# Performance work log

Hardware: AMD Instinct MI355X
Metric: run time of the kernel (lower is better)

## Reference

```python
import jax, jax.numpy as jnp
import numpy as np

N, T, CIN = 40000, 32, 8
VW = 64          # back_voxelwise_channels
P = 16           # v2b_maxvoxels (voxels stacked per BEV cell)
BEV_H, BEV_W = 496, 432
EPS = 1e-5


def _bn(key, shape):
    # returns stacked (gamma, beta, running_mean, running_var) along axis -2
    k1, k2, k3 = jax.random.split(key, 3)
    g = 1.0 + 0.1 * jax.random.normal(k1, shape, jnp.float32)
    b = 0.1 * jax.random.normal(k2, shape, jnp.float32)
    m = 0.1 * jax.random.normal(k3, shape, jnp.float32)
    v = jnp.ones(shape, jnp.float32)
    return jnp.stack([g, b, m, v], axis=-2)


def setup_inputs() -> dict:
    key = jax.random.key(0)
    ks = jax.random.split(key, 20)
    features = jax.random.normal(ks[0], (N, T, CIN), jnp.float32)
    cy = jax.random.randint(ks[1], (N, 1), 0, BEV_H)
    cx = jax.random.randint(ks[2], (N, 1), 0, BEV_W)
    coors = jnp.concatenate([cy, cx], axis=1).astype(jnp.int32)
    num_voxels = jax.random.randint(ks[3], (N,), 1, T + 1).astype(jnp.int32)

    def w(k, o, i):
        return jax.random.normal(k, (o, i), jnp.float32) / float(np.sqrt(i))

    return dict(
        features=features, coors=coors, num_voxels=num_voxels,
        vfe1_W=w(ks[4], 8, CIN), vfe1_bn=_bn(ks[5], (8,)),
        vfe2_W=w(ks[6], 32, 16), vfe2_bn=_bn(ks[7], (32,)),
        vfe3_W=w(ks[8], 64, 64), vfe3_bn=_bn(ks[9], (64,)),
        vfe4_W=w(ks[10], 64, 64), vfe4_bn=_bn(ks[11], (64,)),
        bfe1_W=jax.random.normal(ks[12], (16, P, P), jnp.float32) / float(np.sqrt(P)),
        bfe1_bn=_bn(ks[13], (16, P)),
        bfe2_W=jax.random.normal(ks[14], (16, 2, P), jnp.float32) / float(np.sqrt(P)),
        bfe2_bn=_bn(ks[15], (16, 2)),
        bfe3_W=w(ks[16], 128, 128), bfe3_bn=_bn(ks[17], (128,)),
    )


def _forward(features, vfe1_W, vfe1_bn, vfe2_W, vfe2_bn, vfe3_W, vfe3_bn,
             vfe4_W, vfe4_bn, bfe1_W, bfe1_bn, bfe2_W, bfe2_bn, bfe3_W, bfe3_bn,
             coors, num_voxels):
    n, t = features.shape[0], features.shape[1]
    f32 = features.dtype
    mask = (jnp.arange(t)[None, :] < num_voxels[:, None]).astype(f32)[..., None]  # [N,T,1]

    def fe(x, W, bn):  # Linear (no bias) + BatchNorm1d (eval) + Mish
        g, b, m, v = bn
        y = x @ W.T
        y = (y - m) * jax.lax.rsqrt(v + EPS) * g + b
        return y * jnp.tanh(jax.nn.softplus(y))

    def vfe(x, W, bn):  # pointwise FE, max-pool over points, concat
        p = fe(x, W, bn)
        agg = jnp.max(p, axis=1, keepdims=True)
        return jnp.concatenate([p, jnp.broadcast_to(agg, p.shape)], axis=2)

    x1 = vfe(features, vfe1_W, vfe1_bn)           # [N,T,16]
    x2 = vfe(x1, vfe2_W, vfe2_bn) * mask          # [N,T,64]
    x3 = fe(x2, vfe3_W, vfe3_bn)
    x4 = fe(x3, vfe4_W, vfe4_bn) * mask + x2
    voxelwise = jnp.max(x4, axis=1)               # [N,64]

    # ---- voxel2bev: group voxels by BEV cell, stack up to P per cell ----
    cell = coors[:, 0] * BEV_W + coors[:, 1]                         # [N]
    ucell, inv = jnp.unique(cell, return_inverse=True, size=n, fill_value=BEV_H * BEV_W)
    order = jnp.argsort(inv)                                          # stable
    inv_sorted = inv[order]
    pos_sorted = jnp.arange(n) - jnp.searchsorted(inv_sorted, inv_sorted, side='left')
    slot = jnp.zeros(n, jnp.int32).at[order].set(pos_sorted.astype(jnp.int32))
    row = jnp.where(slot < P, inv, n)                                 # overflow -> dropped
    bevs = jnp.zeros((n, P, VW), f32).at[row, jnp.minimum(slot, P - 1)].set(
        voxelwise, mode='drop')                                       # [N,P,64]
    counts = jax.ops.segment_sum(jnp.ones(n, jnp.int32), inv, num_segments=n)
    numv = jnp.minimum(counts, P)
    bevcoors = jnp.stack([ucell // BEV_W, ucell % BEV_W], axis=1)     # [N,2]

    # ---- 16 grouped FE stacks over the slot dimension ----
    x0 = bevs.transpose(0, 2, 1).reshape(n, 16, 4, P)                 # [N,16,4,P]
    m2 = (jnp.arange(P)[None, :] < numv[:, None]).astype(f32)[:, None, None, :]
    y = jnp.einsum('ngip,gqp->ngiq', x0, bfe1_W)                      # [N,16,4,P]
    g1, b1, m1, v1 = (bfe1_bn[None, :, i, None, :] for i in range(4))
    y = (y - m1) * jax.lax.rsqrt(v1 + EPS) * g1 + b1
    y = y * jnp.tanh(jax.nn.softplus(y)) * m2
    z = jnp.einsum('ngip,gcp->ngic', y, bfe2_W)                       # [N,16,4,2]
    g2, b2, m2b, v2 = (bfe2_bn[None, :, i, None, :] for i in range(4))
    z = (z - m2b) * jax.lax.rsqrt(v2 + EPS) * g2 + b2
    z = z * jnp.tanh(jax.nn.softplus(z))
    # torch cat along dim=-1 then view -> layout [N, 4, 16, 2] flattened
    x17 = z.transpose(0, 2, 1, 3).reshape(n, 128)
    x18 = fe(x17, bfe3_W, bfe3_bn)
    x19 = fe(x18, bfe3_W, bfe3_bn)   # original applies bfe3 twice (bfe4 unused)

    bevmap = jnp.zeros((BEV_H, BEV_W, 128), f32).at[
        bevcoors[:, 0], bevcoors[:, 1]].set(x19, mode='drop')
    return bevmap.transpose(2, 1, 0)                                  # [128, W, H]


def reference(features, coors, num_voxels, vfe1_W, vfe1_bn, vfe2_W, vfe2_bn,
              vfe3_W, vfe3_bn, vfe4_W, vfe4_bn, bfe1_W, bfe1_bn, bfe2_W, bfe2_bn,
              bfe3_W, bfe3_bn):
    return _forward(features, vfe1_W, vfe1_bn, vfe2_W, vfe2_bn, vfe3_W, vfe3_bn,
                    vfe4_W, vfe4_bn, bfe1_W, bfe1_bn, bfe2_W, bfe2_bn,
                    bfe3_W, bfe3_bn, coors, num_voxels)
```

## Files before the change

kernel.cpp:

```cpp
#include <hip/hip_runtime.h>

#define BEVW 432
#define BEVH 496
#define NCELL (BEVW*BEVH)
#define NVOX  40000
#define EPSB  1e-5f

typedef float f32x2 __attribute__((ext_vector_type(2)));
typedef float f32x4 __attribute__((ext_vector_type(4)));
typedef unsigned int u32x4 __attribute__((ext_vector_type(4)));
typedef short bf16x8 __attribute__((ext_vector_type(8)));

#define REP8_0(M)  M(0) M(1) M(2) M(3) M(4) M(5) M(6) M(7)
#define REP8_8(M)  M(8) M(9) M(10) M(11) M(12) M(13) M(14) M(15)
#define REP8_16(M) M(16) M(17) M(18) M(19) M(20) M(21) M(22) M(23)
#define REP8_24(M) M(24) M(25) M(26) M(27) M(28) M(29) M(30) M(31)
#define REP16_0(M)  REP8_0(M)  REP8_8(M)
#define REP32_0(M) REP16_0(M) REP8_16(M) REP8_24(M)


__device__ __forceinline__ float mishf(float y) {
    float e = __expf(fminf(y, 40.f));
    float n = e * (e + 2.f);
    return y * n * __builtin_amdgcn_rcpf(n + 2.f);
}

template <int CTRL>
__device__ __forceinline__ float dppmaxf(float a) {
    int p = __builtin_amdgcn_update_dpp(0, __float_as_int(a), CTRL, 0xF, 0xF, true);
    return fmaxf(a, __int_as_float(p));
}
#define WMAX32(a) { \
    a = dppmaxf<0xB1>(a); \
    a = dppmaxf<0x4E>(a); \
    a = dppmaxf<0x141>(a); \
    a = dppmaxf<0x140>(a); \
    a = fmaxf(a, __int_as_float(__builtin_amdgcn_ds_swizzle(__float_as_int(a), 0x401F))); }

__device__ __forceinline__ bf16x8 mkbf8(uint a, uint b, uint c, uint d) {
    u32x4 t = {a, b, c, d};
    return __builtin_bit_cast(bf16x8, t);
}

__device__ __forceinline__ uint splitbf(float x) {
    uint rh = __float_as_uint(x) & 0xFFFF0000u;
    float lof = x - __uint_as_float(rh);
    uint ul = __float_as_uint(lof);
    uint rl = (ul + 0x7FFFu + ((ul >> 16) & 1u)) >> 16;
    return (rh >> 16) | (rl << 16);
}

__global__ __launch_bounds__(256) void setup_kernel(
    const float* __restrict__ vbn1, const float* __restrict__ vbn2,
    const float* __restrict__ vbn3, const float* __restrict__ vbn4,
    const float* __restrict__ bbn1, const float* __restrict__ bbn2,
    const float* __restrict__ bbn3, const float* __restrict__ W4,
    const float* __restrict__ W3g,
    float* __restrict__ fold, ushort* __restrict__ w4fh, ushort* __restrict__ w4fl,
    ushort* __restrict__ w3fh, ushort* __restrict__ w3fl)
{
    int tid = threadIdx.x;
    if (tid < 8)  { float s = vbn1[tid]/sqrtf(vbn1[24+tid]+EPSB);  fold[tid]      = s; fold[8+tid]   = vbn1[8+tid]  - vbn1[16+tid]*s; }
    if (tid < 32) { float s = vbn2[tid]/sqrtf(vbn2[96+tid]+EPSB);  fold[16+tid]   = s; fold[48+tid]  = vbn2[32+tid] - vbn2[64+tid]*s; }
    if (tid < 64) { float s = vbn3[tid]/sqrtf(vbn3[192+tid]+EPSB); fold[80+tid]   = s; fold[144+tid] = vbn3[64+tid] - vbn3[128+tid]*s; }
    if (tid < 64) { float s = vbn4[tid]/sqrtf(vbn4[192+tid]+EPSB); fold[208+tid]  = s; fold[272+tid] = vbn4[64+tid] - vbn4[128+tid]*s; }
    if (tid < 128){ float s = bbn3[tid]/sqrtf(bbn3[384+tid]+EPSB); fold[336+tid]  = s; fold[464+tid] = bbn3[128+tid]- bbn3[256+tid]*s; }
    { int g = tid >> 4, q = tid & 15;
      const float* b = bbn1 + g*64;
      float s = b[q]/sqrtf(b[48+q]+EPSB);
      fold[592+tid] = s; fold[848+tid] = b[16+q] - b[32+q]*s; }
    if (tid < 32) { int g = tid >> 1, c = tid & 1;
      const float* b = bbn2 + g*8;
      float s = b[c]/sqrtf(b[6+c]+EPSB);
      fold[1104+tid] = s; fold[1136+tid] = b[2+c] - b[4+c]*s; }

    for (int i = tid; i < 4096; i += 256) {
        int j = i & 7, ln = (i >> 3) & 63, nt = (i >> 9) & 3, kc = i >> 11;
        int n = (ln & 15) + nt*16;
        int k = kc*32 + (ln >> 4)*8 + j;
        {
            float val = W4[n*64 + k];
            uint rh = __float_as_uint(val) & 0xFFFF0000u;
            float lof = val - __uint_as_float(rh);
            uint ul = __float_as_uint(lof);
            uint rl = (ul + 0x7FFFu + ((ul >> 16) & 1u)) >> 16;
            w4fh[i] = (ushort)(rh >> 16);
            w4fl[i] = (ushort)rl;
        }
        {
            float val = W3g[n*64 + k];
            uint rh = __float_as_uint(val) & 0xFFFF0000u;
            float lof = val - __uint_as_float(rh);
            uint ul = __float_as_uint(lof);
            uint rl = (ul + 0x7FFFu + ((ul >> 16) & 1u)) >> 16;
            w3fh[i] = (ushort)(rh >> 16);
            w3fl[i] = (ushort)rl;
        }
    }
}

#define PAIRS(M) M(0,0,1) M(1,2,3) M(2,4,5) M(3,6,7) M(4,8,9) M(5,10,11) \
  M(6,12,13) M(7,14,15) M(8,16,17) M(9,18,19) M(10,20,21) M(11,22,23) \
  M(12,24,25) M(13,26,27) M(14,28,29) M(15,30,31)

#define MF3(D, AH, AL, BH, BL) \
    D = __builtin_amdgcn_mfma_f32_16x16x32_bf16(AL, BH, D, 0, 0, 0); \
    D = __builtin_amdgcn_mfma_f32_16x16x32_bf16(AH, BL, D, 0, 0, 0); \
    D = __builtin_amdgcn_mfma_f32_16x16x32_bf16(AH, BH, D, 0, 0, 0);

#define LDA(SRCP, mt, AH, AL) { \
    const uint* ap_ = (SRCP) + ((lane & 15) + 16*(mt))*33 + quad*8; \
    uint u0 = ap_[0], u1 = ap_[1], u2 = ap_[2], u3 = ap_[3]; \
    uint u4 = ap_[4], u5 = ap_[5], u6 = ap_[6], u7 = ap_[7]; \
    AH = mkbf8(__builtin_amdgcn_perm(u1,u0,0x05040100), __builtin_amdgcn_perm(u3,u2,0x05040100), \
               __builtin_amdgcn_perm(u5,u4,0x05040100), __builtin_amdgcn_perm(u7,u6,0x05040100)); \
    AL = mkbf8(__builtin_amdgcn_perm(u1,u0,0x07060302), __builtin_amdgcn_perm(u3,u2,0x07060302), \
               __builtin_amdgcn_perm(u5,u4,0x07060302), __builtin_amdgcn_perm(u7,u6,0x07060302)); }

#define TILE4(SRCP, mt, D0, D1, D2, D3) { \
    bf16x8 Ah_, Al_; LDA(SRCP, mt, Ah_, Al_) \
    MF3(D0, Ah_, Al_, B0h_, B0l_) MF3(D1, Ah_, Al_, B1h_, B1l_) \
    MF3(D2, Ah_, Al_, B2h_, B2l_) MF3(D3, Ah_, Al_, B3h_, B3l_) }

#define DOSET(SRCP, BHP, BLP, ACC, SKA, SKB) { \
    uint4 h0_=(BHP)[0], l0_=(BLP)[0], h1_=(BHP)[64], l1_=(BLP)[64]; \
    uint4 h2_=(BHP)[128], l2_=(BLP)[128], h3_=(BHP)[192], l3_=(BLP)[192]; \
    bf16x8 B0h_=mkbf8(h0_.x,h0_.y,h0_.z,h0_.w), B0l_=mkbf8(l0_.x,l0_.y,l0_.z,l0_.w); \
    bf16x8 B1h_=mkbf8(h1_.x,h1_.y,h1_.z,h1_.w), B1l_=mkbf8(l1_.x,l1_.y,l1_.z,l1_.w); \
    bf16x8 B2h_=mkbf8(h2_.x,h2_.y,h2_.z,h2_.w), B2l_=mkbf8(l2_.x,l2_.y,l2_.z,l2_.w); \
    bf16x8 B3h_=mkbf8(h3_.x,h3_.y,h3_.z,h3_.w), B3l_=mkbf8(l3_.x,l3_.y,l3_.z,l3_.w); \
    TILE4(SRCP, 0, ACC[0], ACC[1], ACC[2], ACC[3]) \
    TILE4(SRCP, 2, ACC[8], ACC[9], ACC[10], ACC[11]) \
    if (!(SKA)) { TILE4(SRCP, 1, ACC[4], ACC[5], ACC[6], ACC[7]) } \
    if (!(SKB)) { TILE4(SRCP, 3, ACC[12], ACC[13], ACC[14], ACC[15]) } }

__global__ __launch_bounds__(64, 3) void vfe_kernel(
    const float* __restrict__ feat, const int* __restrict__ coors,
    const int* __restrict__ nvx,
    const float* __restrict__ W1, const float* __restrict__ W2,
    const ushort* __restrict__ w3fh, const ushort* __restrict__ w3fl,
    const ushort* __restrict__ w4fh, const ushort* __restrict__ w4fl,
    const float* __restrict__ fold,
    float* __restrict__ voxelwise, int* __restrict__ cnt,
    int* __restrict__ list, int* __restrict__ nact, int* __restrict__ act)
{
    __shared__ char ldsbuf[17152];
    int tid = threadIdx.x;
    int lane = tid;
    int quad = lane >> 4;
    int v = blockIdx.x * 2 + (tid >> 5);
    int vA = blockIdx.x * 2;
    int t = tid & 31;
    uint*  x2s  = (uint*)ldsbuf;
    float* aggL = (float*)(ldsbuf + 16896);

    const float* fp = feat + (v*32 + t)*8;
    float4 fa = *(const float4*)fp;
    float4 fb = *(const float4*)(fp+4);
    int numv = nvx[v];
    float maskf = (t < numv) ? 1.f : 0.f;

#define D1(o) float x1_##o; float m1_##o;
    REP8_0(D1)
#undef D1
#define FE1(o) { const float* w = W1 + (o)*8; \
    float ya = fa.x*w[0] + fa.y*w[1]; float yb = fa.z*w[2] + fa.w*w[3]; \
    float yc = fb.x*w[4] + fb.y*w[5]; float yd = fb.z*w[6] + fb.w*w[7]; \
    float yy = ((ya+yb)+(yc+yd)) * fold[(o)] + fold[8+(o)]; \
    x1_##o = mishf(yy); }
    REP8_0(FE1)
#undef FE1
#define P1(o) { float a = x1_##o; WMAX32(a); m1_##o = a; }
    REP8_0(P1)
#undef P1

    f32x2 x1p_0 = {x1_0,x1_1}, x1p_1 = {x1_2,x1_3}, x1p_2 = {x1_4,x1_5}, x1p_3 = {x1_6,x1_7};
    f32x2 m1p_0 = {m1_0,m1_1}, m1p_1 = {m1_2,m1_3}, m1p_2 = {m1_4,m1_5}, m1p_3 = {m1_6,m1_7};

#define D2(o) float x2_##o; float agg_##o;
    REP32_0(D2)
#undef D2
#define FE2(o) { const f32x2* wp = (const f32x2*)(W2 + (o)*16); \
    f32x2 sa = x1p_0*wp[0]; sa += x1p_1*wp[1]; \
    f32x2 sb = x1p_2*wp[2]; sb += x1p_3*wp[3]; \
    f32x2 sc = m1p_0*wp[4]; sc += m1p_1*wp[5]; \
    f32x2 sd = m1p_2*wp[6]; sd += m1p_3*wp[7]; \
    sa += sb; sc += sd; sa += sc; \
    float yy = (sa.x + sa.y) * fold[16+(o)] + fold[48+(o)]; \
    x2_##o = mishf(yy); }
    REP32_0(FE2)
#undef FE2
#define P2(o) { float a = x2_##o; WMAX32(a); agg_##o = a; }
    REP32_0(P2)
#undef P2

#define PX(i,a,b) f32x2 x2p_##i = {x2_##a, x2_##b}; f32x2 aggp_##i = {agg_##a, agg_##b};
    PAIRS(PX)
#undef PX

    f32x2 maskp = {maskf, maskf};
#define MSK(i) x2p_##i *= maskp; aggp_##i *= maskp;
    REP16_0(MSK)
#undef MSK

    if (t == 0) {
        float* ag = aggL + (lane >> 5)*32;
#define AGW(i) ag[2*(i)] = aggp_##i.x; ag[2*(i)+1] = aggp_##i.y;
        REP16_0(AGW)
#undef AGW
    }

    int nA = __builtin_amdgcn_readfirstlane(__shfl(numv, 0));
    int nB = __builtin_amdgcn_readfirstlane(__shfl(numv, 32));
    const bool skipA = (nA <= 16);
    const bool skipB = (nB <= 16);

#define X2W(i) { \
    x2s[lane*33 + 2*(i)]          = splitbf(x2p_##i.x); \
    x2s[lane*33 + 2*(i)+1]        = splitbf(x2p_##i.y); \
    x2s[2112 + lane*33 + 2*(i)]   = splitbf(aggp_##i.x); \
    x2s[2112 + lane*33 + 2*(i)+1] = splitbf(aggp_##i.y); }
    REP16_0(X2W)
#undef X2W

    f32x4 e[16];
#define EIN(i) e[i] = (f32x4){0.f,0.f,0.f,0.f};
    REP16_0(EIN)
#undef EIN
    {
        const uint4* bh3 = (const uint4*)w3fh + lane;
        const uint4* bl3 = (const uint4*)w3fl + lane;
        DOSET(x2s, bh3, bl3, e, skipA, skipB)
    }
    {
        const uint4* bh3 = (const uint4*)w3fh + 256 + lane;
        const uint4* bl3 = (const uint4*)w3fl + 256 + lane;
        const uint* sp = x2s + 2112;
        DOSET(sp, bh3, bl3, e, skipA, skipB)
    }

    int c0 = lane & 15;
    uint* x3st = x2s + 2112;
    f32x4 d[16];
#define DIN(i) d[i] = (f32x4){0.f,0.f,0.f,0.f};
    REP16_0(DIN)
#undef DIN

#define POST(TI, mt, nt) { \
    float s_ = fold[80 + c0 + 16*(nt)], tb_ = fold[144 + c0 + 16*(nt)]; \
    int col_ = c0 + 16*((nt)&1); \
    int rowb_ = quad*4 + 16*(mt); \
    x3st[(rowb_+0)*33 + col_] = splitbf(mishf(e[TI].x * s_ + tb_)); \
    x3st[(rowb_+1)*33 + col_] = splitbf(mishf(e[TI].y * s_ + tb_)); \
    x3st[(rowb_+2)*33 + col_] = splitbf(mishf(e[TI].z * s_ + tb_)); \
    x3st[(rowb_+3)*33 + col_] = splitbf(mishf(e[TI].w * s_ + tb_)); }

    {
        POST(0,0,0)  POST(1,0,1)
        POST(8,2,0)  POST(9,2,1)
        if (!skipA) { POST(4,1,0)  POST(5,1,1) }
        if (!skipB) { POST(12,3,0) POST(13,3,1) }
        const uint4* bh4 = (const uint4*)w4fh + lane;
        const uint4* bl4 = (const uint4*)w4fl + lane;
        DOSET(x3st, bh4, bl4, d, skipA, skipB)
    }
    {
        POST(2,0,2)  POST(3,0,3)
        POST(10,2,2) POST(11,2,3)
        if (!skipA) { POST(6,1,2)  POST(7,1,3) }
        if (!skipB) { POST(14,3,2) POST(15,3,3) }
        const uint4* bh4 = (const uint4*)w4fh + 256 + lane;
        const uint4* bl4 = (const uint4*)w4fl + 256 + lane;
        DOSET(x3st, bh4, bl4, d, skipA, skipB)
    }
#undef POST

    float s0f = fold[208+c0],    t0f = fold[272+c0];
    float s1f = fold[208+16+c0], t1f = fold[272+16+c0];
    float s2f = fold[208+32+c0], t2f = fold[272+32+c0];
    float s3f = fold[208+48+c0], t3f = fold[272+48+c0];
    float rA2 = aggL[c0],      rA3 = aggL[16+c0];
    float rB2 = aggL[32+c0],   rB3 = aggL[48+c0];
    float piA = skipA ? 0.f : -3.4e38f;
    float piB = skipB ? 0.f : -3.4e38f;
    float pA0=piA, pA1=piA, pA2=piA, pA3=piA;
    float pB0=piB, pB1=piB, pB2=piB, pB3=piB;

#define RECON(u) (__uint_as_float((u)<<16) + __uint_as_float((u) & 0xFFFF0000u))
#define FTP(D, mt, nt, SS, TT, PV) { \
    int nv = ((mt) >> 1) ? nB : nA; \
    int rf = quad*4 + 16*(mt); \
    int rt = quad*4 + 16*((mt)&1); \
    int cb = c0 + 16*(nt); \
    float m0=(rt+0<nv)?1.f:0.f, m1=(rt+1<nv)?1.f:0.f, m2=(rt+2<nv)?1.f:0.f, m3=(rt+3<nv)?1.f:0.f; \
    uint ua_ = x2s[(rf+0)*33 + cb], ub_ = x2s[(rf+1)*33 + cb]; \
    uint uc_ = x2s[(rf+2)*33 + cb], ud_ = x2s[(rf+3)*33 + cb]; \
    float y0 = mishf(D.x*SS + TT)*m0 + RECON(ua_); \
    float y1 = mishf(D.y*SS + TT)*m1 + RECON(ub_); \
    float y2 = mishf(D.z*SS + TT)*m2 + RECON(uc_); \
    float y3 = mishf(D.w*SS + TT)*m3 + RECON(ud_); \
    PV = fmaxf(PV, fmaxf(fmaxf(y0,y1), fmaxf(y2,y3))); }

#define FTA(D, mt, nt, SS, TT, AG, PV) { \
    int nv = ((mt) >> 1) ? nB : nA; \
    int rt = quad*4 + 16*((mt)&1); \
    float m0=(rt+0<nv)?1.f:0.f, m1=(rt+1<nv)?1.f:0.f, m2=(rt+2<nv)?1.f:0.f, m3=(rt+3<nv)?1.f:0.f; \
    float y0 = (mishf(D.x*SS + TT) + AG)*m0; \
    float y1 = (mishf(D.y*SS + TT) + AG)*m1; \
    float y2 = (mishf(D.z*SS + TT) + AG)*m2; \
    float y3 = (mishf(D.w*SS + TT) + AG)*m3; \
    PV = fmaxf(PV, fmaxf(fmaxf(y0,y1), fmaxf(y2,y3))); }

    FTP(d[0], 0, 0, s0f, t0f, pA0)  FTP(d[1], 0, 1, s1f, t1f, pA1)
    FTA(d[2], 0, 2, s2f, t2f, rA2, pA2)  FTA(d[3], 0, 3, s3f, t3f, rA3, pA3)
    if (!skipA) {
        FTP(d[4], 1, 0, s0f, t0f, pA0)  FTP(d[5], 1, 1, s1f, t1f, pA1)
        FTA(d[6], 1, 2, s2f, t2f, rA2, pA2)  FTA(d[7], 1, 3, s3f, t3f, rA3, pA3)
    }
    FTP(d[8], 2, 0, s0f, t0f, pB0)  FTP(d[9], 2, 1, s1f, t1f, pB1)
    FTA(d[10], 2, 2, s2f, t2f, rB2, pB2)  FTA(d[11], 2, 3, s3f, t3f, rB3, pB3)
    if (!skipB) {
        FTP(d[12], 3, 0, s0f, t0f, pB0)  FTP(d[13], 3, 1, s1f, t1f, pB1)
        FTA(d[14], 3, 2, s2f, t2f, rB2, pB2)  FTA(d[15], 3, 3, s3f, t3f, rB3, pB3)
    }
#undef FTP
#undef FTA
#undef RECON

#define RED(p) p = fmaxf(p, __shfl_xor(p, 16)); p = fmaxf(p, __shfl_xor(p, 32));
    RED(pA0) RED(pA1) RED(pA2) RED(pA3) RED(pB0) RED(pB1) RED(pB2) RED(pB3)
#undef RED

    if (quad == 0) {
        float* vwA = voxelwise + vA*64;
        vwA[c0] = pA0; vwA[c0+16] = pA1; vwA[c0+32] = pA2; vwA[c0+48] = pA3;
        float* vwB = voxelwise + (vA+1)*64;
        vwB[c0] = pB0; vwB[c0+16] = pB1; vwB[c0+32] = pB2; vwB[c0+48] = pB3;
    }

    if (t == 0) {
        int cell = coors[v*2] * BEVW + coors[v*2+1];
        int pos = atomicAdd(&cnt[cell], 1);
        if (pos < 16) list[cell*16 + pos] = v;
        if (pos == 0) { int k = atomicAdd(nact, 1); act[k] = cell; }
    }
}

__global__ __launch_bounds__(256) void bfe_front(
    const int* __restrict__ nact, const int* __restrict__ act,
    const int* __restrict__ cnt, const int* __restrict__ list,
    const float* __restrict__ voxelwise,
    const float* __restrict__ W1g, const float* __restrict__ W2g,
    const float* __restrict__ fold, float* __restrict__ x17g,
    int* __restrict__ idx)
{
    int n_act = *nact;
    int aidx = blockIdx.x * 4 + (threadIdx.x >> 6);
    if (aidx >= n_act) return;

    int lane = threadIdx.x & 63;
    int g = lane >> 2, ii = lane & 3;
    int cell = act[aidx];
    int numv = min(cnt[cell], 16);
    if (lane == 0) idx[cell] = aidx + 1;

    int myidx = (lane < numv) ? list[cell*16 + lane] : (0x40000000 + lane);
    int rank = 0;
    for (int j = 0; j < numv; j++) { int vj = __shfl(myidx, j); rank += (vj < myidx) ? 1 : 0; }
    if (lane >= numv) rank = lane;
    int sorted = __builtin_amdgcn_ds_permute(rank << 2, myidx);

#define YD(q) float y_##q = 0.f;
    REP16_0(YD)
#undef YD
    for (int p = 0; p < numv; p++) {
        int sv = __shfl(sorted, p);
        float val = voxelwise[sv*64 + lane];
        const float* w = W1g + g*256 + p;
#define BF1(q) y_##q += val * w[(q)*16];
        REP16_0(BF1)
#undef BF1
    }
#define BN1(q) { float yy = y_##q * fold[592 + g*16 + (q)] + fold[848 + g*16 + (q)]; \
    yy = mishf(yy); y_##q = ((q) < numv) ? yy : 0.f; }
    REP16_0(BN1)
#undef BN1

    float z0 = 0.f, z1 = 0.f;
#define BF2(p) z0 += y_##p * W2g[g*32 + (p)]; z1 += y_##p * W2g[g*32 + 16 + (p)];
    REP16_0(BF2)
#undef BF2
    z0 = mishf(z0 * fold[1104 + g*2 + 0] + fold[1136 + g*2 + 0]);
    z1 = mishf(z1 * fold[1104 + g*2 + 1] + fold[1136 + g*2 + 1]);

    int k0 = ii*32 + g*2;
    *(float2*)(x17g + aidx*128 + k0) = make_float2(z0, z1);
}

__global__ __launch_bounds__(512, 4) void bfe3_fused(
    const int* __restrict__ nactp,
    const float* __restrict__ W3, const float* __restrict__ fold,
    float* __restrict__ x17g)
{
    __shared__ float XL[64*128];
    int tid = threadIdx.x;
    int n_act = *nactp;
    int cb = blockIdx.x * 64;

    for (int i = tid; i < 64*32; i += 512) {
        int c = i >> 5, kc = i & 31;
        float4 val = (cb + c < n_act) ? ((const float4*)x17g)[(size_t)(cb+c)*32 + kc]
                                      : make_float4(0.f,0.f,0.f,0.f);
        ((float4*)XL)[c*32 + (kc ^ (c & 31))] = val;
    }
    __syncthreads();

    int wv = __builtin_amdgcn_readfirstlane(tid >> 6);
    int c  = tid & 63;
    int ob = wv * 16;
    int cswz = c & 31;
    const float4* xrow = (const float4*)XL + c*32;
    const float4* W4p = (const float4*)W3;

#define DECLB(q) f32x2 ap_##q = {0.f, 0.f};
#define ACCB(q) { const f32x2* wp_ = (const f32x2*)(W4p + (ob+(q))*32 + kc); \
    ap_##q += xv01 * wp_[0]; ap_##q += xv23 * wp_[1]; }
#define ACTB(q) float a_##q; { float yy = (ap_##q.x + ap_##q.y) * fold[336+ob+(q)] + fold[464+ob+(q)]; a_##q = mishf(yy); }
    {
        REP16_0(DECLB)
        for (int kc = 0; kc < 32; kc++) {
            float4 xv = xrow[kc ^ cswz];
            f32x2 xv01 = {xv.x, xv.y}, xv23 = {xv.z, xv.w};
            REP16_0(ACCB)
        }
        REP16_0(ACTB)
        __syncthreads();
        ((float4*)XL)[c*32 + ((wv*4 + 0) ^ cswz)] = make_float4(a_0,  a_1,  a_2,  a_3);
        ((float4*)XL)[c*32 + ((wv*4 + 1) ^ cswz)] = make_float4(a_4,  a_5,  a_6,  a_7);
        ((float4*)XL)[c*32 + ((wv*4 + 2) ^ cswz)] = make_float4(a_8,  a_9,  a_10, a_11);
        ((float4*)XL)[c*32 + ((wv*4 + 3) ^ cswz)] = make_float4(a_12, a_13, a_14, a_15);
    }
    __syncthreads();

    {
        const float4* yrow = (const float4*)XL + c*32;
        REP16_0(DECLB)
        for (int kc = 0; kc < 32; kc++) {
            float4 xv = yrow[kc ^ cswz];
            f32x2 xv01 = {xv.x, xv.y}, xv23 = {xv.z, xv.w};
            REP16_0(ACCB)
        }
        REP16_0(ACTB)
        float4* dst = (float4*)(x17g + (size_t)(cb + c)*128 + ob);
        dst[0] = make_float4(a_0,  a_1,  a_2,  a_3);
        dst[1] = make_float4(a_4,  a_5,  a_6,  a_7);
        dst[2] = make_float4(a_8,  a_9,  a_10, a_11);
        dst[3] = make_float4(a_12, a_13, a_14, a_15);
    }
#undef DECLB
#undef ACCB
#undef ACTB
}

__global__ __launch_bounds__(512, 2) void bev_write(
    const int* __restrict__ idx, const float* __restrict__ x19c,
    float* __restrict__ out)
{
    __shared__ float XT[128*65];
    int bid = blockIdx.x;
    int cx = bid % BEVW;
    int cy0 = (bid / BEVW) << 6;
    int tid = threadIdx.x;

    int cell_l = tid >> 3;
    int chq = (tid & 7) << 4;
    int cy = cy0 + cell_l;
    float4 v0 = make_float4(0.f,0.f,0.f,0.f), v1 = v0, v2 = v0, v3 = v0;
    if (cy < BEVH) {
        int ai = idx[cy*BEVW + cx] - 1;
        if (ai >= 0) {
            const float4* src = (const float4*)(x19c + (size_t)ai*128 + chq);
            v0 = src[0]; v1 = src[1]; v2 = src[2]; v3 = src[3];
        }
    }
    float* d = XT + chq*65 + cell_l;
    d[0*65]=v0.x;  d[1*65]=v0.y;  d[2*65]=v0.z;  d[3*65]=v0.w;
    d[4*65]=v1.x;  d[5*65]=v1.y;  d[6*65]=v1.z;  d[7*65]=v1.w;
    d[8*65]=v2.x;  d[9*65]=v2.y;  d[10*65]=v2.z; d[11*65]=v2.w;
    d[12*65]=v3.x; d[13*65]=v3.y; d[14*65]=v3.z; d[15*65]=v3.w;
    __syncthreads();

    int wv2 = tid >> 6, lane = tid & 63;
    int cyw = cy0 + lane;
    if (cyw < BEVH) {
        float* op = out + cx*BEVH + cyw;
#pragma unroll
        for (int k = 0; k < 16; k++) {
            int c = (wv2 << 4) + k;
            op[(size_t)c*NCELL] = XT[c*65 + lane];
        }
    }
}

extern "C" void kernel_launch(void* const* d_in, const int* in_sizes, int n_in,
                              void* d_out, int out_size, void* d_ws, size_t ws_size,
                              hipStream_t stream) {
    const float* features = (const float*)d_in[0];
    const int*   coors    = (const int*)d_in[1];
    const int*   num_vox  = (const int*)d_in[2];
    const float* vfe1_W   = (const float*)d_in[3];
    const float* vfe1_bn  = (const float*)d_in[4];
    const float* vfe2_W   = (const float*)d_in[5];
    const float* vfe2_bn  = (const float*)d_in[6];
    const float* vfe3_W   = (const float*)d_in[7];
    const float* vfe3_bn  = (const float*)d_in[8];
    const float* vfe4_W   = (const float*)d_in[9];
    const float* vfe4_bn  = (const float*)d_in[10];
    const float* bfe1_W   = (const float*)d_in[11];
    const float* bfe1_bn  = (const float*)d_in[12];
    const float* bfe2_W   = (const float*)d_in[13];
    const float* bfe2_bn  = (const float*)d_in[14];
    const float* bfe3_W   = (const float*)d_in[15];
    const float* bfe3_bn  = (const float*)d_in[16];
    float* out = (float*)d_out;

    char* ws = (char*)d_ws;
    int*    nact      = (int*)ws;
    int*    cnt       = (int*)(ws + 256);
    int*    idx       = (int*)(ws + 857344);
    int*    list      = (int*)(ws + 1714432);
    float*  voxelwise = (float*)(ws + 15427840);
    int*    act       = (int*)(ws + 25667840);
    float*  x17g      = (float*)(ws + 25827840);
    float*  fold      = (float*)(ws + 46307840);
    ushort* w4fh      = (ushort*)(ws + 46312512);
    ushort* w4fl      = (ushort*)(ws + 46320704);
    ushort* w3fh      = (ushort*)(ws + 46328896);
    ushort* w3fl      = (ushort*)(ws + 46337088);

    (void)hipMemsetAsync(ws, 0, 1714432, stream);

    setup_kernel<<<1, 256, 0, stream>>>(vfe1_bn, vfe2_bn, vfe3_bn, vfe4_bn,
                                        bfe1_bn, bfe2_bn, bfe3_bn, vfe4_W, vfe3_W,
                                        fold, w4fh, w4fl, w3fh, w3fl);
    vfe_kernel<<<NVOX/2, 64, 0, stream>>>(features, coors, num_vox,
                                          vfe1_W, vfe2_W, w3fh, w3fl, w4fh, w4fl, fold,
                                          voxelwise, cnt, list, nact, act);
    bfe_front<<<NVOX/4, 256, 0, stream>>>(nact, act, cnt, list, voxelwise,
                                          bfe1_W, bfe2_W, fold, x17g, idx);
    bfe3_fused<<<(NVOX+63)/64, 512, 0, stream>>>(nact, bfe3_W, fold, x17g);
    bev_write<<<BEVW*8, 512, 0, stream>>>(idx, x17g, out);
}
```

Baseline: 515.0 us.

## Move VFE layer-2 matmul onto split-bf16 MFMA and reduce max via shuffles

Replaces the scalar per-thread 16->32 FMA chain for the second VFE layer with split-bf16 (hi/lo) MFMA tiles. The weights are pre-split in the setup kernel, and the input is staged in LDS as a K=32 padded tile. The per-voxel max aggregation now uses quad-level shuffles on the MFMA output layout instead of DPP wave reductions. Masked x2 and broadcast aggregate values are written directly into the LDS layout used by the next layer. This cuts VALU work but adds LDS round-trips, and three MFMAs with half-zero padding, for a small matmul.

```diff
diff --git a/kernel.cpp b/kernel.cpp
--- a/kernel.cpp
+++ b/kernel.cpp
@@ -13,10 +13,7 @@
 
 #define REP8_0(M)  M(0) M(1) M(2) M(3) M(4) M(5) M(6) M(7)
 #define REP8_8(M)  M(8) M(9) M(10) M(11) M(12) M(13) M(14) M(15)
-#define REP8_16(M) M(16) M(17) M(18) M(19) M(20) M(21) M(22) M(23)
-#define REP8_24(M) M(24) M(25) M(26) M(27) M(28) M(29) M(30) M(31)
 #define REP16_0(M)  REP8_0(M)  REP8_8(M)
-#define REP32_0(M) REP16_0(M) REP8_16(M) REP8_24(M)
 
 
 __device__ __forceinline__ float mishf(float y) {
@@ -55,9 +52,10 @@
     const float* __restrict__ vbn3, const float* __restrict__ vbn4,
     const float* __restrict__ bbn1, const float* __restrict__ bbn2,
     const float* __restrict__ bbn3, const float* __restrict__ W4,
-    const float* __restrict__ W3g,
+    const float* __restrict__ W3g, const float* __restrict__ W2g,
     float* __restrict__ fold, ushort* __restrict__ w4fh, ushort* __restrict__ w4fl,
-    ushort* __restrict__ w3fh, ushort* __restrict__ w3fl)
+    ushort* __restrict__ w3fh, ushort* __restrict__ w3fl,
+    ushort* __restrict__ w2fh, ushort* __restrict__ w2fl)
 {
     int tid = threadIdx.x;
     if (tid < 8)  { float s = vbn1[tid]/sqrtf(vbn1[24+tid]+EPSB);  fold[tid]      = s; fold[8+tid]   = vbn1[8+tid]  - vbn1[16+tid]*s; }
@@ -80,28 +78,28 @@
         int k = kc*32 + (ln >> 4)*8 + j;
         {
             float val = W4[n*64 + k];
-            uint rh = __float_as_uint(val) & 0xFFFF0000u;
-            float lof = val - __uint_as_float(rh);
-            uint ul = __float_as_uint(lof);
-            uint rl = (ul + 0x7FFFu + ((ul >> 16) & 1u)) >> 16;
-            w4fh[i] = (ushort)(rh >> 16);
-            w4fl[i] = (ushort)rl;
+            uint u = splitbf(val);
+            w4fh[i] = (ushort)(u & 0xFFFFu);
+            w4fl[i] = (ushort)(u >> 16);
         }
         {
             float val = W3g[n*64 + k];
-            uint rh = __float_as_uint(val) & 0xFFFF0000u;
-            float lof = val - __uint_as_float(rh);
-            uint ul = __float_as_uint(lof);
-            uint rl = (ul + 0x7FFFu + ((ul >> 16) & 1u)) >> 16;
-            w3fh[i] = (ushort)(rh >> 16);
-            w3fl[i] = (ushort)rl;
+            uint u = splitbf(val);
+            w3fh[i] = (ushort)(u & 0xFFFFu);
+            w3fl[i] = (ushort)(u >> 16);
         }
     }
-}
-
-#define PAIRS(M) M(0,0,1) M(1,2,3) M(2,4,5) M(3,6,7) M(4,8,9) M(5,10,11) \
-  M(6,12,13) M(7,14,15) M(8,16,17) M(9,18,19) M(10,20,21) M(11,22,23) \
-  M(12,24,25) M(13,26,27) M(14,28,29) M(15,30,31)
+
+    for (int i = tid; i < 1024; i += 256) {
+        int j = i & 7, ln = (i >> 3) & 63, nt = (i >> 9) & 1;
+        int n = (ln & 15) + nt*16;
+        int k = (ln >> 4)*8 + j;
+        float val = (k < 16) ? W2g[n*16 + k] : 0.f;
+        uint u = splitbf(val);
+        w2fh[i] = (ushort)(u & 0xFFFFu);
+        w2fl[i] = (ushort)(u >> 16);
+    }
+}
 
 #define MF3(D, AH, AL, BH, BL) \
     D = __builtin_amdgcn_mfma_f32_16x16x32_bf16(AL, BH, D, 0, 0, 0); \
@@ -110,6 +108,15 @@
 
 #define LDA(SRCP, mt, AH, AL) { \
     const uint* ap_ = (SRCP) + ((lane & 15) + 16*(mt))*33 + quad*8; \
+    uint u0 = ap_[0], u1 = ap_[1], u2 = ap_[2], u3 = ap_[3]; \
+    uint u4 = ap_[4], u5 = ap_[5], u6 = ap_[6], u7 = ap_[7]; \
+    AH = mkbf8(__builtin_amdgcn_perm(u1,u0,0x05040100), __builtin_amdgcn_perm(u3,u2,0x05040100), \
+               __builtin_amdgcn_perm(u5,u4,0x05040100), __builtin_amdgcn_perm(u7,u6,0x05040100)); \
+    AL = mkbf8(__builtin_amdgcn_perm(u1,u0,0x07060302), __builtin_amdgcn_perm(u3,u2,0x07060302), \
+               __builtin_amdgcn_perm(u5,u4,0x07060302), __builtin_amdgcn_perm(u7,u6,0x07060302)); }
+
+#define LDA2(SRCP, mt, AH, AL) { \
+    const uint* ap_ = (SRCP) + ((lane & 15) + 16*(mt))*33 + (quad & 1)*8; \
     uint u0 = ap_[0], u1 = ap_[1], u2 = ap_[2], u3 = ap_[3]; \
     uint u4 = ap_[4], u5 = ap_[5], u6 = ap_[6], u7 = ap_[7]; \
     AH = mkbf8(__builtin_amdgcn_perm(u1,u0,0x05040100), __builtin_amdgcn_perm(u3,u2,0x05040100), \
@@ -137,7 +144,8 @@
 __global__ __launch_bounds__(64, 3) void vfe_kernel(
     const float* __restrict__ feat, const int* __restrict__ coors,
     const int* __restrict__ nvx,
-    const float* __restrict__ W1, const float* __restrict__ W2,
+    const float* __restrict__ W1,
+    const ushort* __restrict__ w2fh, const ushort* __restrict__ w2fl,
     const ushort* __restrict__ w3fh, const ushort* __restrict__ w3fl,
     const ushort* __restrict__ w4fh, const ushort* __restrict__ w4fl,
     const float* __restrict__ fold,
@@ -148,17 +156,18 @@
     int tid = threadIdx.x;
     int lane = tid;
     int quad = lane >> 4;
+    int c0 = lane & 15;
     int v = blockIdx.x * 2 + (tid >> 5);
     int vA = blockIdx.x * 2;
     int t = tid & 31;
     uint*  x2s  = (uint*)ldsbuf;
+    uint*  x2s1 = x2s + 2112;
     float* aggL = (float*)(ldsbuf + 16896);
 
     const float* fp = feat + (v*32 + t)*8;
-    float4 fa = *(const float4*)fp;
+    float4 fa = *(const float4*)(fp);
     float4 fb = *(const float4*)(fp+4);
     int numv = nvx[v];
-    float maskf = (t < numv) ? 1.f : 0.f;
 
 #define D1(o) float x1_##o; float m1_##o;
     REP8_0(D1)
@@ -174,54 +183,74 @@
     REP8_0(P1)
 #undef P1
 
-    f32x2 x1p_0 = {x1_0,x1_1}, x1p_1 = {x1_2,x1_3}, x1p_2 = {x1_4,x1_5}, x1p_3 = {x1_6,x1_7};
-    f32x2 m1p_0 = {m1_0,m1_1}, m1p_1 = {m1_2,m1_3}, m1p_2 = {m1_4,m1_5}, m1p_3 = {m1_6,m1_7};
-
-#define D2(o) float x2_##o; float agg_##o;
-    REP32_0(D2)
-#undef D2
-#define FE2(o) { const f32x2* wp = (const f32x2*)(W2 + (o)*16); \
-    f32x2 sa = x1p_0*wp[0]; sa += x1p_1*wp[1]; \
-    f32x2 sb = x1p_2*wp[2]; sb += x1p_3*wp[3]; \
-    f32x2 sc = m1p_0*wp[4]; sc += m1p_1*wp[5]; \
-    f32x2 sd = m1p_2*wp[6]; sd += m1p_3*wp[7]; \
-    sa += sb; sc += sd; sa += sc; \
-    float yy = (sa.x + sa.y) * fold[16+(o)] + fold[48+(o)]; \
-    x2_##o = mishf(yy); }
-    REP32_0(FE2)
-#undef FE2
-#define P2(o) { float a = x2_##o; WMAX32(a); agg_##o = a; }
-    REP32_0(P2)
-#undef P2
-
-#define PX(i,a,b) f32x2 x2p_##i = {x2_##a, x2_##b}; f32x2 aggp_##i = {agg_##a, agg_##b};
-    PAIRS(PX)
-#undef PX
-
-    f32x2 maskp = {maskf, maskf};
-#define MSK(i) x2p_##i *= maskp; aggp_##i *= maskp;
-    REP16_0(MSK)
-#undef MSK
-
-    if (t == 0) {
-        float* ag = aggL + (lane >> 5)*32;
-#define AGW(i) ag[2*(i)] = aggp_##i.x; ag[2*(i)+1] = aggp_##i.y;
-        REP16_0(AGW)
-#undef AGW
-    }
-
     int nA = __builtin_amdgcn_readfirstlane(__shfl(numv, 0));
     int nB = __builtin_amdgcn_readfirstlane(__shfl(numv, 32));
     const bool skipA = (nA <= 16);
     const bool skipB = (nB <= 16);
 
-#define X2W(i) { \
-    x2s[lane*33 + 2*(i)]          = splitbf(x2p_##i.x); \
-    x2s[lane*33 + 2*(i)+1]        = splitbf(x2p_##i.y); \
-    x2s[2112 + lane*33 + 2*(i)]   = splitbf(aggp_##i.x); \
-    x2s[2112 + lane*33 + 2*(i)+1] = splitbf(aggp_##i.y); }
-    REP16_0(X2W)
-#undef X2W
+#define S1(o) { x2s1[lane*33 + (o)] = splitbf(x1_##o); x2s1[lane*33 + 8 + (o)] = splitbf(m1_##o); }
+    REP8_0(S1)
+#undef S1
+
+    f32x4 f2[8];
+#pragma unroll
+    for (int i = 0; i < 8; i++) f2[i] = (f32x4){0.f,0.f,0.f,0.f};
+    {
+        const uint4* bh2 = (const uint4*)w2fh + lane;
+        const uint4* bl2 = (const uint4*)w2fl + lane;
+        uint4 h0_=bh2[0], l0_=bl2[0], h1_=bh2[64], l1_=bl2[64];
+        bf16x8 B0h_=mkbf8(h0_.x,h0_.y,h0_.z,h0_.w), B0l_=mkbf8(l0_.x,l0_.y,l0_.z,l0_.w);
+        bf16x8 B1h_=mkbf8(h1_.x,h1_.y,h1_.z,h1_.w), B1l_=mkbf8(l1_.x,l1_.y,l1_.z,l1_.w);
+        { bf16x8 Ah_,Al_; LDA2(x2s1,0,Ah_,Al_) MF3(f2[0],Ah_,Al_,B0h_,B0l_) MF3(f2[1],Ah_,Al_,B1h_,B1l_) }
+        { bf16x8 Ah_,Al_; LDA2(x2s1,1,Ah_,Al_) MF3(f2[2],Ah_,Al_,B0h_,B0l_) MF3(f2[3],Ah_,Al_,B1h_,B1l_) }
+        { bf16x8 Ah_,Al_; LDA2(x2s1,2,Ah_,Al_) MF3(f2[4],Ah_,Al_,B0h_,B0l_) MF3(f2[5],Ah_,Al_,B1h_,B1l_) }
+        { bf16x8 Ah_,Al_; LDA2(x2s1,3,Ah_,Al_) MF3(f2[6],Ah_,Al_,B0h_,B0l_) MF3(f2[7],Ah_,Al_,B1h_,B1l_) }
+    }
+
+    float s2a = fold[16+c0], t2a = fold[48+c0];
+    float s2b = fold[32+c0], t2b = fold[64+c0];
+#define MSH4(s, SS, TT) { f2[s].x=mishf(f2[s].x*(SS)+(TT)); f2[s].y=mishf(f2[s].y*(SS)+(TT)); \
+                          f2[s].z=mishf(f2[s].z*(SS)+(TT)); f2[s].w=mishf(f2[s].w*(SS)+(TT)); }
+    MSH4(0,s2a,t2a) MSH4(1,s2b,t2b) MSH4(2,s2a,t2a) MSH4(3,s2b,t2b)
+    MSH4(4,s2a,t2a) MSH4(5,s2b,t2b) MSH4(6,s2a,t2a) MSH4(7,s2b,t2b)
+#undef MSH4
+
+#define MX4(V) fmaxf(fmaxf((V).x,(V).y), fmaxf((V).z,(V).w))
+    float aggA0 = fmaxf(MX4(f2[0]), MX4(f2[2]));
+    float aggA1 = fmaxf(MX4(f2[1]), MX4(f2[3]));
+    float aggB0 = fmaxf(MX4(f2[4]), MX4(f2[6]));
+    float aggB1 = fmaxf(MX4(f2[5]), MX4(f2[7]));
+#undef MX4
+#define REDQ(p) p = fmaxf(p, __shfl_xor(p, 16)); p = fmaxf(p, __shfl_xor(p, 32));
+    REDQ(aggA0) REDQ(aggA1) REDQ(aggB0) REDQ(aggB1)
+#undef REDQ
+    if (lane < 16) {
+        aggL[c0]    = aggA0;  aggL[16+c0] = aggA1;
+        aggL[32+c0] = aggB0;  aggL[48+c0] = aggB1;
+    }
+    uint sgA0 = splitbf(aggA0), sgA1 = splitbf(aggA1);
+    uint sgB0 = splitbf(aggB0), sgB1 = splitbf(aggB1);
+
+#define ST2(mt, NVV, SG0, SG1) { \
+    int rt_ = quad*4 + 16*((mt)&1); \
+    int gr_ = (quad*4 + 16*(mt))*33; \
+    float m0_=(rt_+0<(NVV))?1.f:0.f, m1_=(rt_+1<(NVV))?1.f:0.f; \
+    float m2_=(rt_+2<(NVV))?1.f:0.f, m3_=(rt_+3<(NVV))?1.f:0.f; \
+    f32x4 a_ = f2[(mt)*2], b_ = f2[(mt)*2+1]; \
+    x2s[gr_    + c0] = splitbf(a_.x*m0_);  x2s[gr_    + c0+16] = splitbf(b_.x*m0_); \
+    x2s[gr_+33 + c0] = splitbf(a_.y*m1_);  x2s[gr_+33 + c0+16] = splitbf(b_.y*m1_); \
+    x2s[gr_+66 + c0] = splitbf(a_.z*m2_);  x2s[gr_+66 + c0+16] = splitbf(b_.z*m2_); \
+    x2s[gr_+99 + c0] = splitbf(a_.w*m3_);  x2s[gr_+99 + c0+16] = splitbf(b_.w*m3_); \
+    x2s1[gr_    + c0] = (m0_!=0.f)?(SG0):0u;  x2s1[gr_    + c0+16] = (m0_!=0.f)?(SG1):0u; \
+    x2s1[gr_+33 + c0] = (m1_!=0.f)?(SG0):0u;  x2s1[gr_+33 + c0+16] = (m1_!=0.f)?(SG1):0u; \
+    x2s1[gr_+66 + c0] = (m2_!=0.f)?(SG0):0u;  x2s1[gr_+66 + c0+16] = (m2_!=0.f)?(SG1):0u; \
+    x2s1[gr_+99 + c0] = (m3_!=0.f)?(SG0):0u;  x2s1[gr_+99 + c0+16] = (m3_!=0.f)?(SG1):0u; }
+    ST2(0, nA, sgA0, sgA1)
+    ST2(2, nB, sgB0, sgB1)
+    if (!skipA) { ST2(1, nA, sgA0, sgA1) }
+    if (!skipB) { ST2(3, nB, sgB0, sgB1) }
+#undef ST2
+
 
     f32x4 e[16];
 #define EIN(i) e[i] = (f32x4){0.f,0.f,0.f,0.f};
@@ -235,12 +264,11 @@
     {
         const uint4* bh3 = (const uint4*)w3fh + 256 + lane;
         const uint4* bl3 = (const uint4*)w3fl + 256 + lane;
-        const uint* sp = x2s + 2112;
+        const uint* sp = x2s1;
         DOSET(sp, bh3, bl3, e, skipA, skipB)
     }
 
-    int c0 = lane & 15;
-    uint* x3st = x2s + 2112;
+    uint* x3st = x2s1;
     f32x4 d[16];
 #define DIN(i) d[i] = (f32x4){0.f,0.f,0.f,0.f};
     REP16_0(DIN)
@@ -537,14 +565,16 @@
     ushort* w4fl      = (ushort*)(ws + 46320704);
     ushort* w3fh      = (ushort*)(ws + 46328896);
     ushort* w3fl      = (ushort*)(ws + 46337088);
+    ushort* w2fh      = (ushort*)(ws + 46345280);
+    ushort* w2fl      = (ushort*)(ws + 46347328);
 
     (void)hipMemsetAsync(ws, 0, 1714432, stream);
 
     setup_kernel<<<1, 256, 0, stream>>>(vfe1_bn, vfe2_bn, vfe3_bn, vfe4_bn,
-                                        bfe1_bn, bfe2_bn, bfe3_bn, vfe4_W, vfe3_W,
-                                        fold, w4fh, w4fl, w3fh, w3fl);
+                                        bfe1_bn, bfe2_bn, bfe3_bn, vfe4_W, vfe3_W, vfe2_W,
+                                        fold, w4fh, w4fl, w3fh, w3fl, w2fh, w2fl);
     vfe_kernel<<<NVOX/2, 64, 0, stream>>>(features, coors, num_vox,
-                                          vfe1_W, vfe2_W, w3fh, w3fl, w4fh, w4fl, fold,
+                                          vfe1_W, w2fh, w2fl, w3fh, w3fl, w4fh, w4fl, fold,
                                           voxelwise, cnt, list, nact, act);
     bfe_front<<<NVOX/4, 256, 0, stream>>>(nact, act, cnt, list, voxelwise,
                                           bfe1_W, bfe2_W, fold, x17g, idx);
```

Measured after the change: 508.9 us. Within noise of the previous version (-1.2%).
